# Optimization experiments

Hardware: AMD Instinct MI355X
Metric: run time of the kernel (lower is better)

Reference implementation:

```python
import jax, jax.numpy as jnp
import numpy as np

B, T, D, I, C, H = 8192, 128, 7, 128, 10, 64
L = 2 ** D
SUBSET = int(I * 0.8)  # feature_subset_size = 102


def setup_inputs() -> dict:
    key = jax.random.key(0)
    ks = jax.random.split(key, 7)
    x = jax.random.normal(ks[0], (B, I), dtype=jnp.float32)
    # exact feature-subset mask: SUBSET ones per (tree, depth) row
    r = jax.random.uniform(ks[1], (T, D, I))
    ranks = jnp.argsort(jnp.argsort(r, axis=-1), axis=-1)
    feature_mask = (ranks < SUBSET).astype(jnp.float32)
    thresholds = jax.random.normal(ks[2], (T, D), dtype=jnp.float32)
    leaf_outputs = jax.random.normal(ks[3], (T, L, C), dtype=jnp.float32)
    W1 = jax.random.normal(ks[4], (I, H), dtype=jnp.float32) * 0.08
    b1 = jnp.zeros((H,), dtype=jnp.float32)
    W2 = jax.random.normal(ks[5], (H, T), dtype=jnp.float32) * 0.12
    b2 = jnp.zeros((T,), dtype=jnp.float32)
    return {"x": x, "feature_mask": feature_mask, "thresholds": thresholds,
            "leaf_outputs": leaf_outputs, "W1": W1, "b1": b1, "W2": W2, "b2": b2}


def reference(x, feature_mask, thresholds, leaf_outputs, W1, b1, W2, b2):
    depth = thresholds.shape[1]
    # split logits: masked feature sum minus threshold, per (batch, tree, depth)
    z = jnp.einsum('bi,tdi->btd', x, feature_mask) - thresholds[None, :, :]
    s = 0.5 * (z / (1.0 + jnp.abs(z)) + 1.0)  # scaled softsign split in (0,1)
    # probabilistic path routing: doubling concat, identical to torch loop
    p = jnp.ones((x.shape[0], feature_mask.shape[0], 1), dtype=x.dtype)
    for d in range(depth):
        sd = s[:, :, d:d + 1]            # [B, T, 1]
        p = jnp.concatenate([p * sd, p * (1.0 - sd)], axis=-1)  # [B, T, 2^(d+1)]
    leaf_probs = jax.nn.softmax(leaf_outputs, axis=-1)           # [T, L, C]
    tree_outputs = jnp.einsum('btl,tlc->btc', p, leaf_probs)     # [B, T, C]
    # instance-wise attention over trees (eval mode: no dropout)
    attn = jax.nn.softmax(jax.nn.relu(x @ W1 + b1) @ W2 + b2, axis=-1)  # [B, T]
    return jnp.sum(tree_outputs * attn[:, :, None], axis=1)     # [B, C]
```

## Files before the change

kernel.cpp:

```cpp
#include <hip/hip_runtime.h>
#include <hip/hip_bf16.h>
#include <hip/hip_fp16.h>


#define BB 8192
#define TT 128
#define II 128
#define CC 10
#define HH 64

#define OFF_LPB 524288
#define OFF_XBF 606208
#define OFF_MBF 1130496

typedef __attribute__((ext_vector_type(8))) short short8;
typedef __attribute__((ext_vector_type(16))) float floatx16;

static __device__ inline unsigned int pkbf(float lo, float hi) {
  __hip_bfloat162 h = __float22bfloat162_rn(make_float2(lo, hi));
  unsigned int u;
  __builtin_memcpy(&u, &h, 4);
  return u;
}

static __device__ inline unsigned int pkh(float lo, float hi) {
  __half2 h = __float22half2_rn(make_float2(lo, hi));
  unsigned int u;
  __builtin_memcpy(&u, &h, 4);
  return u;
}

static __device__ inline short8 cvt8(float4 a, float4 b) {
  union { short8 v; unsigned int u[4]; } r;
  r.u[0] = pkbf(a.x, a.y);
  r.u[1] = pkbf(a.z, a.w);
  r.u[2] = pkbf(b.x, b.y);
  r.u[3] = pkbf(b.z, b.w);
  return r.v;
}

__global__ __launch_bounds__(256, 2) void prep_kernel(
    const float* __restrict__ x, const float* __restrict__ mask,
    const float* __restrict__ lo,
    const float* __restrict__ W1, const float* __restrict__ b1,
    const float* __restrict__ W2, const float* __restrict__ b2,
    __half* __restrict__ attnB, unsigned int* __restrict__ lpbG,
    unsigned short* __restrict__ xbf, unsigned short* __restrict__ mbf,
    float* __restrict__ out) {
  __shared__ __align__(16) char smem_raw[18432];
  const int blk = blockIdx.x;
  const int tid = threadIdx.x;
  const int wv = tid >> 6, lane = tid & 63;
  const int half = lane >> 5, l31 = lane & 31;

  if (blk < 64) {
    const int b0 = blk * 128 + wv * 32;

    short8 axf[8];
    const float* xrow = x + (size_t)(b0 + l31) * II + half * 8;
#pragma unroll
    for (int s = 0; s < 8; ++s)
      axf[s] = cvt8(*(const float4*)(xrow + s * 16),
                    *(const float4*)(xrow + s * 16 + 4));

    floatx16 acch[2];
#pragma unroll
    for (int i = 0; i < 16; ++i) { acch[0][i] = 0.f; acch[1][i] = 0.f; }
#pragma unroll
    for (int s = 0; s < 8; ++s) {
#pragma unroll
      for (int tile = 0; tile < 2; ++tile) {
        union { short8 v; unsigned int u[4]; } wf;
#pragma unroll
        for (int jp = 0; jp < 4; ++jp) {
          int k0 = s * 16 + half * 8 + jp * 2;
          float f0 = W1[(size_t)k0 * HH + tile * 32 + l31];
          float f1 = W1[(size_t)(k0 + 1) * HH + tile * 32 + l31];
          wf.u[jp] = pkbf(f0, f1);
        }
        acch[tile] = __builtin_amdgcn_mfma_f32_32x32x16_bf16(
            axf[s], wf.v, acch[tile], 0, 0, 0);
      }
    }
    __hip_bfloat16* hids = (__hip_bfloat16*)smem_raw + wv * (32 * 72);
#pragma unroll
    for (int tile = 0; tile < 2; ++tile) {
      float bh = b1[tile * 32 + l31];
#pragma unroll
      for (int r = 0; r < 16; ++r) {
        int row = (r & 3) + 8 * (r >> 2) + 4 * half;
        hids[row * 72 + tile * 32 + l31] =
            __float2bfloat16(fmaxf(acch[tile][r] + bh, 0.f));
      }
    }
    __syncthreads();

    short8 ahf[4];
#pragma unroll
    for (int s = 0; s < 4; ++s)
      ahf[s] = *(const short8*)(hids + l31 * 72 + s * 16 + half * 8);

    floatx16 accl[4];
#pragma unroll
    for (int tile = 0; tile < 4; ++tile) {
#pragma unroll
      for (int i = 0; i < 16; ++i) accl[tile][i] = 0.f;
#pragma unroll
      for (int s = 0; s < 4; ++s) {
        union { short8 v; unsigned int u[4]; } wf;
#pragma unroll
        for (int jp = 0; jp < 4; ++jp) {
          int k0 = s * 16 + half * 8 + jp * 2;
          float f0 = W2[(size_t)k0 * TT + tile * 32 + l31];
          float f1 = W2[(size_t)(k0 + 1) * TT + tile * 32 + l31];
          wf.u[jp] = pkbf(f0, f1);
        }
        accl[tile] = __builtin_amdgcn_mfma_f32_32x32x16_bf16(
            ahf[s], wf.v, accl[tile], 0, 0, 0);
      }
      float bt = b2[tile * 32 + l31];
#pragma unroll
      for (int i = 0; i < 16; ++i) accl[tile][i] += bt;
    }

    float mrow[16];
#pragma unroll
    for (int r = 0; r < 16; ++r)
      mrow[r] = fmaxf(fmaxf(accl[0][r], accl[1][r]),
                      fmaxf(accl[2][r], accl[3][r]));
#pragma unroll
    for (int msk = 1; msk <= 16; msk <<= 1)
#pragma unroll
      for (int r = 0; r < 16; ++r)
        mrow[r] = fmaxf(mrow[r], __shfl_xor(mrow[r], msk, 64));
    float srow[16];
#pragma unroll
    for (int r = 0; r < 16; ++r) srow[r] = 0.f;
#pragma unroll
    for (int tile = 0; tile < 4; ++tile)
#pragma unroll
      for (int r = 0; r < 16; ++r) {
        float e = __expf(accl[tile][r] - mrow[r]);
        accl[tile][r] = e;
        srow[r] += e;
      }
#pragma unroll
    for (int msk = 1; msk <= 16; msk <<= 1)
#pragma unroll
      for (int r = 0; r < 16; ++r)
        srow[r] += __shfl_xor(srow[r], msk, 64);
#pragma unroll
    for (int r = 0; r < 16; ++r) srow[r] = 1.f / srow[r];

#pragma unroll
    for (int tile = 0; tile < 4; ++tile)
#pragma unroll
      for (int r = 0; r < 16; ++r) {
        int row = (r & 3) + 8 * (r >> 2) + 4 * half;
        attnB[(size_t)(b0 + row) * TT + tile * 32 + l31] =
            __float2half(accl[tile][r] * srow[r]);
      }

  } else if (blk < 128) {
    float* lps = (float*)smem_raw;
    const int t0 = (blk - 64) * 2;
    {
      int tl = tid >> 7, l = tid & 127;
      const float* row = lo + ((size_t)(t0 + tl) * 128 + l) * CC;
      float v[CC];
      float m = -1e30f;
#pragma unroll
      for (int c = 0; c < CC; ++c) { v[c] = row[c]; m = fmaxf(m, v[c]); }
      float s = 0.f;
#pragma unroll
      for (int c = 0; c < CC; ++c) { v[c] = __expf(v[c] - m); s += v[c]; }
      float inv = 1.f / s;
      float* o = lps + (tl * 128 + l) * 12;
#pragma unroll
      for (int c = 0; c < CC; ++c) o[c] = v[c] * inv;
    }
    __syncthreads();

#pragma unroll
    for (int jj = 0; jj < 2; ++jj) {
      int idx = jj * 256 + tid;
      if (idx < 320) {
        int tl = idx / 160, rem = idx - tl * 160;
        int s = rem / 20, e = rem - s * 20;
        int n = e >> 1, hf = e & 1;
        unsigned int wd[4];
#pragma unroll
        for (int jp = 0; jp < 4; ++jp) {
          int l0 = s * 16 + hf * 8 + jp * 2;
          float f0 = lps[(tl * 128 + l0) * 12 + n];
          float f1 = lps[(tl * 128 + l0 + 1) * 12 + n];
          wd[jp] = pkh(f0, f1);
        }
        ((uint4*)lpbG)[(size_t)(t0 + tl) * 160 + s * 20 + n * 2 + hf] =
            make_uint4(wd[0], wd[1], wd[2], wd[3]);
      }
    }
  } else if (blk < 199) {
    const float* src;
    unsigned short* dst;
    size_t base;
    if (blk < 192) { src = x;    dst = xbf; base = (size_t)(blk - 128) * 16384; }
    else           { src = mask; dst = mbf; base = (size_t)(blk - 192) * 16384; }
#pragma unroll
    for (int j = 0; j < 8; ++j) {
      size_t e = base + (size_t)j * 2048 + (size_t)tid * 8;
      float4 a = *(const float4*)(src + e);
      float4 b = *(const float4*)(src + e + 4);
      *(short8*)(dst + e) = cvt8(a, b);
    }
  } else {
    ((float4*)out)[(blk - 199) * 256 + tid] = make_float4(0.f, 0.f, 0.f, 0.f);
  }
}

__global__ __launch_bounds__(256, 6) void main_kernel(
    const unsigned short* __restrict__ xbf, const unsigned short* __restrict__ mbf,
    const float* __restrict__ thr, const __half* __restrict__ attnB,
    const unsigned int* __restrict__ lpbG, float* __restrict__ out) {
  __shared__ __align__(16) char smem_raw[16384];
  const int tid = threadIdx.x;
  const int wv = tid >> 6, lane = tid & 63;
  const int half = lane >> 5, l31 = lane & 31;
  const int phys = blockIdx.x;
  const int bg2 = (phys & 7) + ((phys >> 7) << 3);
  const int tg  = (phys >> 3) & 15;
  const int bl = wv * 32 + l31;

  __half* zsl = (__half*)smem_raw;

  __half av[8];
  *(uint4*)av = ((const uint4*)attnB)[(size_t)(bg2 * 128 + bl) * 16 + tg];

  {
    const int m0 = tg * 56;
    short8 xf[8];
    const unsigned short* xr = xbf + (size_t)(bg2 * 128 + bl) * II + half * 8;
#pragma unroll
    for (int s = 0; s < 8; ++s) xf[s] = *(const short8*)(xr + s * 16);

#pragma unroll
    for (int tile = 0; tile < 2; ++tile) {
      int mr = m0 + tile * 28 + l31; if (mr > 895) mr = 895;
      const unsigned short* mrow = mbf + (size_t)mr * II + half * 8;
      short8 af[8];
#pragma unroll
      for (int s = 0; s < 8; ++s) af[s] = *(const short8*)(mrow + s * 16);
      float th[16];
#pragma unroll
      for (int r = 0; r < 16; ++r) {
        int row = (r & 3) + 8 * (r >> 2) + 4 * half;
        int mrr = m0 + tile * 28 + row;
        th[r] = thr[mrr > 895 ? 895 : mrr];
      }
      floatx16 acc;
#pragma unroll
      for (int i = 0; i < 16; ++i) acc[i] = 0.f;
#pragma unroll
      for (int s = 0; s < 8; ++s)
        acc = __builtin_amdgcn_mfma_f32_32x32x16_bf16(af[s], xf[s], acc, 0, 0, 0);

#pragma unroll
      for (int r = 0; r < 16; ++r) {
        int row = (r & 3) + 8 * (r >> 2) + 4 * half;
        if (row < 28) {
          int tl = row / 7;
          int d = row - tl * 7;
          float z = acc[r] - th[r];
          float o = 0.5f * (z / (1.f + fabsf(z)) + 1.f);
          zsl[((tl + tile * 4) * 128 + bl) * 8 + d] = __float2half(o);
        }
      }
    }
  }

  {
    const uint4* zsl4 = (const uint4*)smem_raw;
    const uint4* lpt = (const uint4*)lpbG + (size_t)tg * 1280;

    floatx16 acc;
#pragma unroll
    for (int i = 0; i < 16; ++i) acc[i] = 0.f;

#pragma unroll
    for (int it = 0; it < 8; ++it) {
      uint4 bf[8];
#pragma unroll
      for (int s = 0; s < 8; ++s)
        bf[s] = (l31 < CC) ? lpt[(it * 8 + s) * 20 + l31 * 2 + half]
                           : make_uint4(0u, 0u, 0u, 0u);
      uint4 sv = zsl4[it * 128 + bl];

      const __half* sh = (const __half*)&sv;
      float s0 = __half2float(sh[0]), s1 = __half2float(sh[1]);
      float s2 = __half2float(sh[2]), s3 = __half2float(sh[3]);
      float s4 = __half2float(sh[4]), s5 = __half2float(sh[5]);
      float s6 = __half2float(sh[6]);
      float A  = __half2float(av[it]);

      float s0c = 1.f - s0, s1c = 1.f - s1, s2c = 1.f - s2;
      float t0 = s0 * s1, t1 = s0c * s1, t2 = s0 * s1c, t3 = s0c * s1c;
      float pl[8];
      pl[0] = t0 * s2;  pl[1] = t1 * s2;  pl[2] = t2 * s2;  pl[3] = t3 * s2;
      pl[4] = t0 * s2c; pl[5] = t1 * s2c; pl[6] = t2 * s2c; pl[7] = t3 * s2c;
      float sel3 = half ? (1.f - s3) : s3;
      float Af = A * sel3;
      float s4c = 1.f - s4, s5c = 1.f - s5;
      float as6 = Af * s6, as6c = Af * (1.f - s6);
      float u0 = s4 * s5, u1 = s4c * s5, u2 = s4 * s5c, u3 = s4c * s5c;
      float wv8[8];
      wv8[0] = u0 * as6;  wv8[1] = u1 * as6;
      wv8[2] = u2 * as6;  wv8[3] = u3 * as6;
      wv8[4] = u0 * as6c; wv8[5] = u1 * as6c;
      wv8[6] = u2 * as6c; wv8[7] = u3 * as6c;
      __half2 pl2[4];
#pragma unroll
      for (int jp = 0; jp < 4; ++jp)
        pl2[jp] = __float22half2_rn(make_float2(pl[jp * 2], pl[jp * 2 + 1]));

#pragma unroll
      for (int s = 0; s < 8; ++s) {
        union { short8 v; __half2 h[4]; } a0;
        __half2 w2 = __half2half2(__float2half(wv8[s]));
#pragma unroll
        for (int jp = 0; jp < 4; ++jp) a0.h[jp] = __hmul2(pl2[jp], w2);
        acc = __builtin_amdgcn_mfma_f32_32x32x16_f16(
            a0.v, *(const short8*)&bf[s], acc, 0, 0, 0);
      }
    }

    __syncthreads();
    float* red = (float*)smem_raw;
    if (l31 < CC) {
#pragma unroll
      for (int r = 0; r < 16; ++r) {
        int row = (r & 3) + 8 * (r >> 2) + 4 * half;
        red[(wv * 32 + row) * 10 + l31] = acc[r];
      }
    }
    __syncthreads();
#pragma unroll
    for (int j = 0; j < 5; ++j) {
      int idx = tid + 256 * j;
      atomicAdd(out + (size_t)bg2 * 1280 + idx, red[idx]);
    }
  }
}

extern "C" void kernel_launch(void* const* d_in, const int* in_sizes, int n_in,
                              void* d_out, int out_size, void* d_ws, size_t ws_size,
                              hipStream_t stream) {
  const float* x    = (const float*)d_in[0];
  const float* mask = (const float*)d_in[1];
  const float* thr  = (const float*)d_in[2];
  const float* lo   = (const float*)d_in[3];
  const float* W1   = (const float*)d_in[4];
  const float* b1   = (const float*)d_in[5];
  const float* W2   = (const float*)d_in[6];
  const float* b2   = (const float*)d_in[7];
  float* out = (float*)d_out;
  float* ws  = (float*)d_ws;

  __half*        attnB = (__half*)ws;
  unsigned int*  LPb   = (unsigned int*)(ws + OFF_LPB);
  unsigned short* xbf  = (unsigned short*)(ws + OFF_XBF);
  unsigned short* mbf  = (unsigned short*)(ws + OFF_MBF);

  prep_kernel<<<279, 256, 0, stream>>>(x, mask, lo, W1, b1, W2, b2,
                                       attnB, LPb, xbf, mbf, out);
  main_kernel<<<1024, 256, 0, stream>>>(xbf, mbf, thr, attnB, LPb, out);
}
```

Measured before the change: 104.7 us.

## Split prep kernel into single-wave blocks and double-buffer leaf-prob loads

The prep kernel now runs as 708 blocks of one wave each instead of 279 four-wave blocks, so its attention, leaf-softmax, bf16 conversion and output-zeroing work is spread across more CUs. The main kernel's inner loop prefetches the next iteration's leaf-probability fragments into a second register buffer while the current MFMA step runs, overlapping global loads with compute. Occupancy for the main kernel is lowered from 6 to 4 blocks per CU to leave room for the extra registers. The trade-off is higher register pressure and lower occupancy in exchange for better latency hiding.

```diff
diff --git a/kernel.cpp b/kernel.cpp
--- a/kernel.cpp
+++ b/kernel.cpp
@@ -39,7 +39,7 @@
   return r.v;
 }
 
-__global__ __launch_bounds__(256, 2) void prep_kernel(
+__global__ __launch_bounds__(64) void prep_kernel(
     const float* __restrict__ x, const float* __restrict__ mask,
     const float* __restrict__ lo,
     const float* __restrict__ W1, const float* __restrict__ b1,
@@ -47,14 +47,13 @@
     __half* __restrict__ attnB, unsigned int* __restrict__ lpbG,
     unsigned short* __restrict__ xbf, unsigned short* __restrict__ mbf,
     float* __restrict__ out) {
-  __shared__ __align__(16) char smem_raw[18432];
+  __shared__ __align__(16) char smem_raw[6144];
   const int blk = blockIdx.x;
-  const int tid = threadIdx.x;
-  const int wv = tid >> 6, lane = tid & 63;
+  const int lane = threadIdx.x;
   const int half = lane >> 5, l31 = lane & 31;
 
-  if (blk < 64) {
-    const int b0 = blk * 128 + wv * 32;
+  if (blk < 256) {
+    const int b0 = blk * 32;
 
     short8 axf[8];
     const float* xrow = x + (size_t)(b0 + l31) * II + half * 8;
@@ -82,7 +81,7 @@
             axf[s], wf.v, acch[tile], 0, 0, 0);
       }
     }
-    __hip_bfloat16* hids = (__hip_bfloat16*)smem_raw + wv * (32 * 72);
+    __hip_bfloat16* hids = (__hip_bfloat16*)smem_raw;
 #pragma unroll
     for (int tile = 0; tile < 2; ++tile) {
       float bh = b1[tile * 32 + l31];
@@ -161,12 +160,13 @@
             __float2half(accl[tile][r] * srow[r]);
       }
 
-  } else if (blk < 128) {
+  } else if (blk < 384) {
     float* lps = (float*)smem_raw;
-    const int t0 = (blk - 64) * 2;
-    {
-      int tl = tid >> 7, l = tid & 127;
-      const float* row = lo + ((size_t)(t0 + tl) * 128 + l) * CC;
+    const int t0 = blk - 256;
+#pragma unroll
+    for (int rr = 0; rr < 2; ++rr) {
+      int l = lane * 2 + rr;
+      const float* row = lo + ((size_t)t0 * 128 + l) * CC;
       float v[CC];
       float m = -1e30f;
 #pragma unroll
@@ -175,50 +175,52 @@
 #pragma unroll
       for (int c = 0; c < CC; ++c) { v[c] = __expf(v[c] - m); s += v[c]; }
       float inv = 1.f / s;
-      float* o = lps + (tl * 128 + l) * 12;
+      float* o = lps + l * 12;
 #pragma unroll
       for (int c = 0; c < CC; ++c) o[c] = v[c] * inv;
     }
     __syncthreads();
 
 #pragma unroll
-    for (int jj = 0; jj < 2; ++jj) {
-      int idx = jj * 256 + tid;
-      if (idx < 320) {
-        int tl = idx / 160, rem = idx - tl * 160;
-        int s = rem / 20, e = rem - s * 20;
+    for (int jj = 0; jj < 3; ++jj) {
+      int idx = jj * 64 + lane;
+      if (idx < 160) {
+        int s = idx / 20, e = idx - s * 20;
         int n = e >> 1, hf = e & 1;
         unsigned int wd[4];
 #pragma unroll
         for (int jp = 0; jp < 4; ++jp) {
           int l0 = s * 16 + hf * 8 + jp * 2;
-          float f0 = lps[(tl * 128 + l0) * 12 + n];
-          float f1 = lps[(tl * 128 + l0 + 1) * 12 + n];
+          float f0 = lps[l0 * 12 + n];
+          float f1 = lps[(l0 + 1) * 12 + n];
           wd[jp] = pkh(f0, f1);
         }
-        ((uint4*)lpbG)[(size_t)(t0 + tl) * 160 + s * 20 + n * 2 + hf] =
+        ((uint4*)lpbG)[(size_t)t0 * 160 + idx] =
             make_uint4(wd[0], wd[1], wd[2], wd[3]);
       }
     }
-  } else if (blk < 199) {
+  } else if (blk < 668) {
     const float* src;
     unsigned short* dst;
     size_t base;
-    if (blk < 192) { src = x;    dst = xbf; base = (size_t)(blk - 128) * 16384; }
-    else           { src = mask; dst = mbf; base = (size_t)(blk - 192) * 16384; }
+    if (blk < 640) { src = x;    dst = xbf; base = (size_t)(blk - 384) * 4096; }
+    else           { src = mask; dst = mbf; base = (size_t)(blk - 640) * 4096; }
 #pragma unroll
     for (int j = 0; j < 8; ++j) {
-      size_t e = base + (size_t)j * 2048 + (size_t)tid * 8;
+      size_t e = base + (size_t)j * 512 + (size_t)lane * 8;
       float4 a = *(const float4*)(src + e);
       float4 b = *(const float4*)(src + e + 4);
       *(short8*)(dst + e) = cvt8(a, b);
     }
   } else {
-    ((float4*)out)[(blk - 199) * 256 + tid] = make_float4(0.f, 0.f, 0.f, 0.f);
+    const int base4 = (blk - 668) * 512;
+#pragma unroll
+    for (int j = 0; j < 8; ++j)
+      ((float4*)out)[base4 + j * 64 + lane] = make_float4(0.f, 0.f, 0.f, 0.f);
   }
 }
 
-__global__ __launch_bounds__(256, 6) void main_kernel(
+__global__ __launch_bounds__(256, 4) void main_kernel(
     const unsigned short* __restrict__ xbf, const unsigned short* __restrict__ mbf,
     const float* __restrict__ thr, const __half* __restrict__ attnB,
     const unsigned int* __restrict__ lpbG, float* __restrict__ out) {
@@ -286,15 +288,8 @@
 #pragma unroll
     for (int i = 0; i < 16; ++i) acc[i] = 0.f;
 
-#pragma unroll
-    for (int it = 0; it < 8; ++it) {
-      uint4 bf[8];
-#pragma unroll
-      for (int s = 0; s < 8; ++s)
-        bf[s] = (l31 < CC) ? lpt[(it * 8 + s) * 20 + l31 * 2 + half]
-                           : make_uint4(0u, 0u, 0u, 0u);
+    auto dostep = [&](int it, const uint4* bf) {
       uint4 sv = zsl4[it * 128 + bl];
-
       const __half* sh = (const __half*)&sv;
       float s0 = __half2float(sh[0]), s1 = __half2float(sh[1]);
       float s2 = __half2float(sh[2]), s3 = __half2float(sh[3]);
@@ -331,7 +326,24 @@
         acc = __builtin_amdgcn_mfma_f32_32x32x16_f16(
             a0.v, *(const short8*)&bf[s], acc, 0, 0, 0);
       }
-    }
+    };
+
+#define PF(dst, itn)                                                       \
+  _Pragma("unroll") for (int s = 0; s < 8; ++s)                            \
+      dst[s] = (l31 < CC) ? lpt[((itn) * 8 + s) * 20 + l31 * 2 + half]     \
+                          : make_uint4(0u, 0u, 0u, 0u);
+
+    uint4 bf0[8], bf1[8];
+    PF(bf0, 0)
+#pragma unroll
+    for (int ith = 0; ith < 4; ++ith) {
+      const int it = ith * 2;
+      PF(bf1, it + 1)
+      dostep(it, bf0);
+      if (ith < 3) { PF(bf0, it + 2) }
+      dostep(it + 1, bf1);
+    }
+#undef PF
 
     __syncthreads();
     float* red = (float*)smem_raw;
@@ -365,12 +377,12 @@
   float* out = (float*)d_out;
   float* ws  = (float*)d_ws;
 
-  __half*        attnB = (__half*)ws;
-  unsigned int*  LPb   = (unsigned int*)(ws + OFF_LPB);
-  unsigned short* xbf  = (unsigned short*)(ws + OFF_XBF);
-  unsigned short* mbf  = (unsigned short*)(ws + OFF_MBF);
-
-  prep_kernel<<<279, 256, 0, stream>>>(x, mask, lo, W1, b1, W2, b2,
-                                       attnB, LPb, xbf, mbf, out);
+  __half*         attnB = (__half*)ws;
+  unsigned int*   LPb   = (unsigned int*)(ws + OFF_LPB);
+  unsigned short* xbf   = (unsigned short*)(ws + OFF_XBF);
+  unsigned short* mbf   = (unsigned short*)(ws + OFF_MBF);
+
+  prep_kernel<<<708, 64, 0, stream>>>(x, mask, lo, W1, b1, W2, b2,
+                                      attnB, LPb, xbf, mbf, out);
   main_kernel<<<1024, 256, 0, stream>>>(xbf, mbf, thr, attnB, LPb, out);
 }
```

New measurement: 101.7 us. -2.8%, faster.
